# Kernel optimization log

Measured on AMD Instinct MI355X. Metric: run time of the kernel, lower is better.

Reference implementation:

```python
import jax, jax.numpy as jnp
import numpy as np

DIM = 256
HEADS = 8
HID = 4 * DIM
EPS = 1e-5


def _layernorm(x, g, b):
    mu = jnp.mean(x, axis=-1, keepdims=True)
    var = jnp.var(x, axis=-1, keepdims=True)
    return (x - mu) * jax.lax.rsqrt(var + EPS) * g + b


def setup_inputs() -> dict:
    key = jax.random.key(0)
    ks = jax.random.split(key, 16)
    s = 0.02
    return {
        "x": jax.random.normal(ks[0], (8, DIM, 32, 32), jnp.float32),
        "ln1_g": jnp.ones((DIM,), jnp.float32),
        "ln1_b": jnp.zeros((DIM,), jnp.float32),
        "wqkv": jax.random.normal(ks[1], (3 * DIM, DIM), jnp.float32) * s,
        "bqkv": jnp.zeros((3 * DIM,), jnp.float32),
        "wo": jax.random.normal(ks[2], (DIM, DIM), jnp.float32) * s,
        "bo": jnp.zeros((DIM,), jnp.float32),
        "ln2_g": jnp.ones((DIM,), jnp.float32),
        "ln2_b": jnp.zeros((DIM,), jnp.float32),
        "w1": jax.random.normal(ks[3], (HID, DIM), jnp.float32) * s,
        "b1": jnp.zeros((HID,), jnp.float32),
        "w2": jax.random.normal(ks[4], (DIM, HID), jnp.float32) * s,
        "b2": jnp.zeros((DIM,), jnp.float32),
        "c1_w": jax.random.normal(ks[5], (DIM, DIM), jnp.float32) * s,
        "c1_b": jnp.zeros((DIM,), jnp.float32),
        "c2_w": jax.random.normal(ks[6], (DIM, DIM), jnp.float32) * s,
        "c2_b": jnp.zeros((DIM,), jnp.float32),
        "c3_w": jax.random.normal(ks[7], (DIM, DIM), jnp.float32) * s,
        "c3_b": jnp.zeros((DIM,), jnp.float32),
        "dw_w": jax.random.normal(ks[8], (DIM, 1, 3, 3), jnp.float32) * s,
        "dw_b": jnp.zeros((DIM,), jnp.float32),
    }


def _block(x, ln1_g, ln1_b, wqkv, bqkv, wo, bo, ln2_g, ln2_b,
           w1, b1, w2, b2, c1_w, c1_b, c2_w, c2_b, c3_w, c3_b, dw_w, dw_b):
    b, c, h, w = x.shape
    s = h * w
    t = x.reshape(b, c, s).transpose(0, 2, 1)  # [b, s, c]

    # --- MHA sublayer ---
    tn = _layernorm(t, ln1_g, ln1_b)
    qkv = tn @ wqkv.T + bqkv                    # [b, s, 3c]
    q, k, v = jnp.split(qkv, 3, axis=-1)
    d = c // HEADS
    q = q.reshape(b, s, HEADS, d)
    k = k.reshape(b, s, HEADS, d)
    v = v.reshape(b, s, HEADS, d)
    scores = jnp.einsum("bshd,bthd->bhst", q, k) / jnp.sqrt(jnp.float32(d))
    attn = jax.nn.softmax(scores, axis=-1)
    o = jnp.einsum("bhst,bthd->bshd", attn, v).reshape(b, s, c)
    t = t + (o @ wo.T + bo)

    # --- MLP sublayer ---
    tn = _layernorm(t, ln2_g, ln2_b)
    hdn = jax.nn.gelu(tn @ w1.T + b1, approximate=False)
    t = t + (hdn @ w2.T + b2)

    x2 = t.transpose(0, 2, 1).reshape(b, c, h, w)

    # --- FeatureDenoiser: channel-attention ([b,c,c]) + depthwise gaussian ---
    def conv1x1(z, wgt, bias):
        return jnp.einsum("oc,bchw->bohw", wgt, z) + bias[None, :, None, None]

    qf = conv1x1(x2, c1_w, c1_b).reshape(b, c, s)
    kf = conv1x1(x2, c2_w, c2_b).reshape(b, c, s)
    vf = conv1x1(x2, c3_w, c3_b).reshape(b, c, s)
    a = jax.nn.softmax(jnp.einsum("bcs,bds->bcd", qf, kf), axis=-1)  # [b,c,c]
    den = jnp.einsum("bcd,bds->bcs", a, vf).reshape(b, c, h, w)
    local = jax.lax.conv_general_dilated(
        x2, dw_w, window_strides=(1, 1), padding="SAME",
        dimension_numbers=("NCHW", "OIHW", "NCHW"),
        feature_group_count=c) + dw_b[None, :, None, None]
    return x2 + 0.1 * den + 0.1 * local


def reference(x, ln1_g, ln1_b, wqkv, bqkv, wo, bo, ln2_g, ln2_b,
              w1, b1, w2, b2, c1_w, c1_b, c2_w, c2_b, c3_w, c3_b, dw_w, dw_b):
    return _block(x, ln1_g, ln1_b, wqkv, bqkv, wo, bo, ln2_g, ln2_b,
                  w1, b1, w2, b2, c1_w, c1_b, c2_w, c2_b, c3_w, c3_b, dw_w, dw_b)
```

## Files before the change

### kernel.cpp

```cpp
#include <hip/hip_runtime.h>
#include <hip/hip_bf16.h>
#include <math.h>

#define B_   8
#define C_   256
#define S_   1024
#define M_   8192
#define HID_ 1024
#define NELT 2097152

typedef __attribute__((ext_vector_type(4))) float f32x4;
typedef __attribute__((ext_vector_type(8))) short bf16x8;

__device__ __forceinline__ ushort f2bf(float f) {
  union { float f; unsigned u; } c; c.f = f;
  unsigned u = c.u;
  return (ushort)((u + 0x7fff + ((u >> 16) & 1)) >> 16);
}
__device__ __forceinline__ ushort f2bf_fast(float f) {
  __hip_bfloat16 h = __float2bfloat16(f);
  return *reinterpret_cast<ushort*>(&h);
}
__device__ __forceinline__ float bf2f(ushort u) {
  union { unsigned u; float f; } c;
  c.u = ((unsigned)u) << 16;
  return c.f;
}

__device__ __forceinline__ float waveReduceSum(float v) {
#pragma unroll
  for (int off = 32; off > 0; off >>= 1) v += __shfl_xor(v, off);
  return v;
}

__global__ __launch_bounds__(512) void ln1_tiled(const float* __restrict__ x,
                                                 const float* __restrict__ g,
                                                 const float* __restrict__ bta,
                                                 float* __restrict__ t,
                                                 ushort* __restrict__ tn) {
  __shared__ float T[32][257];
  __shared__ float mus[32], rss[32];
  int blk = blockIdx.x;
  int st = blk & 31, b = blk >> 5;
  int tid = threadIdx.x;
  int s0 = st * 32;
  for (int i = tid; i < 2048; i += 512) {
    int c = i >> 3, j4 = (i & 7) * 4;
    float4 v = *(const float4*)&x[((size_t)(b * 256 + c) << 10) + s0 + j4];
    T[j4 + 0][c] = v.x; T[j4 + 1][c] = v.y;
    T[j4 + 2][c] = v.z; T[j4 + 3][c] = v.w;
  }
  __syncthreads();
  {
    int j = tid >> 4, e = tid & 15;
    float s1 = 0.f, s2 = 0.f;
#pragma unroll
    for (int cc = 0; cc < 16; ++cc) {
      float v = T[j][e + cc * 16];
      s1 += v; s2 += v * v;
    }
    s1 += __shfl_xor(s1, 1); s2 += __shfl_xor(s2, 1);
    s1 += __shfl_xor(s1, 2); s2 += __shfl_xor(s2, 2);
    s1 += __shfl_xor(s1, 4); s2 += __shfl_xor(s2, 4);
    s1 += __shfl_xor(s1, 8); s2 += __shfl_xor(s2, 8);
    if (e == 0) {
      float mu = s1 * (1.0f / 256.0f);
      float var = s2 * (1.0f / 256.0f) - mu * mu;
      mus[j] = mu;
      rss[j] = rsqrtf(var + 1e-5f);
    }
  }
  __syncthreads();
  for (int i = tid; i < 4096; i += 512) {
    int jj = i >> 7, c = (i & 127) * 2;
    float mu = mus[jj], rs = rss[jj];
    float v0 = T[jj][c], v1 = T[jj][c + 1];
    size_t row = (size_t)(b * 1024 + s0 + jj) * 256 + c;
    float2 tv = {v0, v1};
    *(float2*)&t[row] = tv;
    uint pk = (uint)f2bf((v0 - mu) * rs * g[c] + bta[c]) |
              ((uint)f2bf((v1 - mu) * rs * g[c + 1] + bta[c + 1]) << 16);
    *(uint*)&tn[row] = pk;
  }
}

__global__ __launch_bounds__(256) void ln_kernel(const float* __restrict__ in,
                                                 const float* __restrict__ g,
                                                 const float* __restrict__ bta,
                                                 ushort* __restrict__ tn) {
  int wave = threadIdx.x >> 6, lane = threadIdx.x & 63;
  int row = blockIdx.x * 4 + wave;
  float4 v = *(const float4*)&in[(size_t)row * 256 + lane * 4];
  float s1 = (v.x + v.y) + (v.z + v.w);
  float s2 = (v.x * v.x + v.y * v.y) + (v.z * v.z + v.w * v.w);
#pragma unroll
  for (int off = 32; off > 0; off >>= 1) {
    s1 += __shfl_xor(s1, off);
    s2 += __shfl_xor(s2, off);
  }
  float mu = s1 * (1.0f / 256.0f);
  float var = s2 * (1.0f / 256.0f) - mu * mu;
  float rs = rsqrtf(var + 1e-5f);
  float4 gv = *(const float4*)&g[lane * 4];
  float4 bv = *(const float4*)&bta[lane * 4];
  uint2 pk;
  pk.x = (uint)f2bf((v.x - mu) * rs * gv.x + bv.x) |
         ((uint)f2bf((v.y - mu) * rs * gv.y + bv.y) << 16);
  pk.y = (uint)f2bf((v.z - mu) * rs * gv.z + bv.z) |
         ((uint)f2bf((v.w - mu) * rs * gv.w + bv.w) << 16);
  *(uint2*)&tn[(size_t)row * 256 + lane * 4] = pk;
}

__global__ __launch_bounds__(256) void cvt_all(
    const float* __restrict__ s0, const float* __restrict__ s1,
    const float* __restrict__ s2, const float* __restrict__ s3,
    const float* __restrict__ s4, const float* __restrict__ s5,
    const float* __restrict__ s6, const float* __restrict__ b0,
    const float* __restrict__ b1, const float* __restrict__ b2,
    ushort* __restrict__ dst, float* __restrict__ dstb) {
  int i = blockIdx.x * 256 + threadIdx.x;
  if (i < 983040) {
    const float* s; int off;
    if (i < 196608)      { s = s0; off = 0; }
    else if (i < 262144) { s = s1; off = 196608; }
    else if (i < 524288) { s = s2; off = 262144; }
    else if (i < 786432) { s = s3; off = 524288; }
    else if (i < 851968) { s = s4; off = 786432; }
    else if (i < 917504) { s = s5; off = 851968; }
    else                 { s = s6; off = 917504; }
    dst[i] = f2bf(s[i - off]);
  } else {
    int j = i - 983040;
    dstb[j] = j < 256 ? b0[j] : (j < 512 ? b1[j - 256] : b2[j - 512]);
  }
}

__device__ __forceinline__ int swzr(int r) { return (r ^ (r >> 2)) & 3; }
__device__ __forceinline__ float gelu_exact(float v) {
  return 0.5f * v * (1.0f + erff(v * 0.70710678118654752f));
}

template <int MF, int ACT, int EPI, int BROW>
__global__ __launch_bounds__(256) void gemm_t(
    const ushort* __restrict__ A, const ushort* __restrict__ W,
    const float* __restrict__ bias, const float* __restrict__ res,
    float* __restrict__ Cf, ushort* __restrict__ Cb, void* __restrict__ Cx,
    void* __restrict__ Cx2, int M, int Nn, int K,
    int a_rpb, long long a_bstride, int w_rpb, long long w_bstride) {
  __shared__ ushort As[MF * 2048];
  __shared__ ushort Bs[2048];
  int tid = threadIdx.x;
  int lane = tid & 63, wave = tid >> 6;
  int m0 = blockIdx.y * (MF * 64), n0 = blockIdx.x * 64;
  int kz = blockIdx.z;
  int Kp = K / (int)gridDim.z;
  int kbeg = kz * Kp;
  if (EPI == 0 && Cf) Cf += (size_t)kz * ((size_t)M * Nn);
  const ushort* Ab;
  if (a_rpb)
    Ab = A + (size_t)(m0 / a_rpb) * a_bstride + (size_t)(m0 % a_rpb) * K;
  else
    Ab = A + (size_t)m0 * K;
  const ushort* Wb = W + (size_t)n0 * K;
  if (w_rpb) Wb += (size_t)(m0 / w_rpb) * w_bstride;
  int srow = tid >> 2;
  int sch = tid & 3;
  int fr = lane & 15, fh = lane >> 4;
  int wr = wave * (MF * 16);
  f32x4 acc[MF][4];
#pragma unroll
  for (int i = 0; i < MF; ++i)
#pragma unroll
    for (int j = 0; j < 4; ++j) acc[i][j] = (f32x4){0.f, 0.f, 0.f, 0.f};

  int sw0 = (sch ^ swzr(srow)) * 8;
  int sw1 = (sch ^ swzr(srow + 64)) * 8;
  for (int k0 = kbeg; k0 < kbeg + Kp; k0 += 32) {
    uint4 a0 = *(const uint4*)&Ab[(size_t)srow * K + k0 + sch * 8];
    uint4 a1;
    if (MF == 2) a1 = *(const uint4*)&Ab[(size_t)(srow + 64) * K + k0 + sch * 8];
    uint4 b0 = *(const uint4*)&Wb[(size_t)srow * K + k0 + sch * 8];
    __syncthreads();
    *(uint4*)&As[srow * 32 + sw0] = a0;
    if (MF == 2) *(uint4*)&As[(srow + 64) * 32 + sw1] = a1;
    *(uint4*)&Bs[srow * 32 + sw0] = b0;
    __syncthreads();
    bf16x8 af[MF], bfv[4];
#pragma unroll
    for (int mi = 0; mi < MF; ++mi) {
      int r = wr + mi * 16 + fr;
      af[mi] = *(const bf16x8*)&As[r * 32 + ((fh ^ swzr(r)) * 8)];
    }
#pragma unroll
    for (int ni = 0; ni < 4; ++ni) {
      int r = ni * 16 + fr;
      bfv[ni] = *(const bf16x8*)&Bs[r * 32 + ((fh ^ swzr(r)) * 8)];
    }
#pragma unroll
    for (int mi = 0; mi < MF; ++mi)
#pragma unroll
      for (int ni = 0; ni < 4; ++ni)
        acc[mi][ni] = __builtin_amdgcn_mfma_f32_16x16x32_bf16(
            af[mi], bfv[ni], acc[mi][ni], 0, 0, 0);
  }
#pragma unroll
  for (int mi = 0; mi < MF; ++mi) {
    int rowb = m0 + wr + mi * 16 + fh * 4;
#pragma unroll
    for (int ni = 0; ni < 4; ++ni) {
      int col = n0 + ni * 16 + fr;
      float bv = 0.f;
      if (bias && !BROW) bv = bias[col];
      float vals[4];
#pragma unroll
      for (int r = 0; r < 4; ++r) {
        int row = rowb + r;
        float v = acc[mi][ni][r];
        if (bias && BROW) bv = bias[row & 255];
        v += bv;
        if (ACT == 1) v = gelu_exact(v);
        if (res) v += res[(size_t)row * Nn + col];
        vals[r] = v;
      }
      if (EPI == 0) {
#pragma unroll
        for (int r = 0; r < 4; ++r)
          Cf[(size_t)(rowb + r) * Nn + col] = vals[r];
      } else if (EPI == 1) {
#pragma unroll
        for (int r = 0; r < 4; ++r)
          Cb[(size_t)(rowb + r) * Nn + col] = f2bf(vals[r]);
      } else if (EPI == 3) {
        int bb = rowb >> 10;
        int s0v = rowb & 1023;
        if (col < 256) {
#pragma unroll
          for (int r = 0; r < 4; ++r)
            Cb[(size_t)(rowb + r) * 256 + col] = f2bf(vals[r]);
        } else if (col < 512) {
          int d = col - 256, hh = d >> 5, dh = d & 31;
          ushort* kfr = (ushort*)Cx;
          size_t base = ((size_t)(bb * 8 + hh) * 64 + (s0v >> 4)) * 512 +
                        (dh >> 3) * 128 + (dh & 7) + (s0v & 15) * 8;
#pragma unroll
          for (int r = 0; r < 4; ++r) kfr[base + r * 8] = f2bf(vals[r]);
        } else {
          int d = col - 512, hh = d >> 5, dh = d & 31;
          int chunk = s0v >> 5, lg = (s0v >> 3) & 3;
          int lr = dh & 15, half = dh >> 4;
          ushort* vfr = (ushort*)Cx2;
          size_t base = ((size_t)(bb * 8 + hh) * 64 + chunk * 2 + half) * 512 +
                        (lr + 16 * lg) * 8 + (s0v & 7);
          uint2 pk;
          pk.x = (uint)f2bf(vals[0]) | ((uint)f2bf(vals[1]) << 16);
          pk.y = (uint)f2bf(vals[2]) | ((uint)f2bf(vals[3]) << 16);
          *(uint2*)&vfr[base] = pk;
        }
      } else if (EPI == 4) {
#pragma unroll
        for (int r = 0; r < 4; ++r)
          Cb[(size_t)(rowb + r) * Nn + col] = f2bf(vals[r]);
        float4 v4 = {vals[0], vals[1], vals[2], vals[3]};
        float* x2p = (float*)Cx;
        *(float4*)&x2p[((size_t)((rowb >> 10) * 256 + col)) * 1024 +
                       (rowb & 1023)] = v4;
      } else if (EPI == 5) {
        if (col < 512) {
          uint2 pk;
          pk.x = (uint)f2bf(vals[0]) | ((uint)f2bf(vals[1]) << 16);
          pk.y = (uint)f2bf(vals[2]) | ((uint)f2bf(vals[3]) << 16);
          ushort* qk = (ushort*)Cx;
          *(uint2*)&qk[(size_t)(col >> 8) * 2097152 +
                       (((size_t)(rowb >> 10) * 256 + (col & 255)) << 10) +
                       (rowb & 1023)] = pk;
        } else {
#pragma unroll
          for (int r = 0; r < 4; ++r)
            Cb[(size_t)(rowb + r) * 256 + (col - 512)] = f2bf(vals[r]);
        }
      }
    }
  }
}

__global__ __launch_bounds__(256, 4) void attn_mfma(const ushort* __restrict__ q_bf,
                                                    const ushort* __restrict__ kfrag,
                                                    const ushort* __restrict__ vfrag,
                                                    ushort* __restrict__ o) {
  __shared__ ushort P[4][16][136];
  int blk = blockIdx.x;
  int qt = (blk >> 3) & 15;
  int bh = ((blk & 7) << 3) | (blk >> 7);
  int b = bh >> 3, h = bh & 7;
  int tid = threadIdx.x, wave = tid >> 6, lane = tid & 63;
  int lr = lane & 15, lg = lane >> 4;
  int q0 = qt * 64 + wave * 16;
  bf16x8 qf = *(const bf16x8*)&q_bf[(size_t)((b << 10) + q0 + lr) * 256 +
                                    h * 32 + lg * 8];
  const ushort* kbase = kfrag + (size_t)bh * 32768 + lane * 8;
  const ushort* vbase = vfrag + (size_t)bh * 32768 + lane * 8;
  ushort* Prow = &P[wave][lr][0];
  int xs = lr & 7;
  f32x4 o0 = {0.f, 0.f, 0.f, 0.f}, o1 = {0.f, 0.f, 0.f, 0.f};
  float lsum = 0.f;
  const float scale = 0.17677669529663687f;
  const f32x4 zero = {0.f, 0.f, 0.f, 0.f};

  bf16x8 kf[8];
#pragma unroll
  for (int i = 0; i < 8; ++i)
    kf[i] = *(const bf16x8*)&kbase[(size_t)i * 512];

  for (int t = 0; t < 8; ++t) {
    f32x4 s[8];
    __builtin_amdgcn_s_setprio(1);
#pragma unroll
    for (int i = 0; i < 8; ++i)
      s[i] = __builtin_amdgcn_mfma_f32_16x16x32_bf16(kf[i], qf, zero, 0, 0, 0);
    __builtin_amdgcn_s_setprio(0);
    bf16x8 v0f[4], v1f[4];
#pragma unroll
    for (int kc = 0; kc < 4; ++kc) {
      v0f[kc] = *(const bf16x8*)&vbase[(size_t)((t * 4 + kc) * 2) * 512];
      v1f[kc] = *(const bf16x8*)&vbase[(size_t)((t * 4 + kc) * 2 + 1) * 512];
    }
    if (t < 7) {
#pragma unroll
      for (int i = 0; i < 8; ++i)
        kf[i] = *(const bf16x8*)&kbase[(size_t)((t + 1) * 8 + i) * 512];
    }
    float ps = 0.f;
#pragma unroll
    for (int i = 0; i < 8; ++i) {
      float p0 = __expf(fminf(s[i][0] * scale, 30.f));
      float p1 = __expf(fminf(s[i][1] * scale, 30.f));
      float p2 = __expf(fminf(s[i][2] * scale, 30.f));
      float p3 = __expf(fminf(s[i][3] * scale, 30.f));
      ps += (p0 + p1) + (p2 + p3);
      uint2 pk;
      pk.x = (uint)f2bf_fast(p0) | ((uint)f2bf_fast(p1) << 16);
      pk.y = (uint)f2bf_fast(p2) | ((uint)f2bf_fast(p3) << 16);
      *(uint2*)&Prow[((i ^ xs) * 16) + lg * 4] = pk;
    }
    lsum += ps;
    __builtin_amdgcn_s_setprio(1);
#pragma unroll
    for (int kc4 = 0; kc4 < 4; ++kc4) {
      bf16x8 pf = *(const bf16x8*)&Prow[((kc4 * 8 + lg * 2) ^ (xs * 4)) * 4];
      o0 = __builtin_amdgcn_mfma_f32_16x16x32_bf16(v0f[kc4], pf, o0, 0, 0, 0);
      o1 = __builtin_amdgcn_mfma_f32_16x16x32_bf16(v1f[kc4], pf, o1, 0, 0, 0);
    }
    __builtin_amdgcn_s_setprio(0);
  }
  float lf = lsum + __shfl_xor(lsum, 16);
  lf += __shfl_xor(lf, 32);
  float inv = 1.f / lf;
  uint2 pk0, pk1;
  pk0.x = (uint)f2bf_fast(o0[0] * inv) | ((uint)f2bf_fast(o0[1] * inv) << 16);
  pk0.y = (uint)f2bf_fast(o0[2] * inv) | ((uint)f2bf_fast(o0[3] * inv) << 16);
  pk1.x = (uint)f2bf_fast(o1[0] * inv) | ((uint)f2bf_fast(o1[1] * inv) << 16);
  pk1.y = (uint)f2bf_fast(o1[2] * inv) | ((uint)f2bf_fast(o1[3] * inv) << 16);
  ushort* orow = &o[(size_t)((b << 10) + q0 + lr) * 256 + h * 32];
  *(uint2*)&orow[lg * 4] = pk0;
  *(uint2*)&orow[16 + lg * 4] = pk1;
}

template <int KS>
__global__ __launch_bounds__(256) void softmax256(const float* __restrict__ a,
                                                  ushort* __restrict__ ab) {
  __shared__ float s1s[4];
  int row = blockIdx.x;
  int j = threadIdx.x;
  float v = 0.f;
#pragma unroll
  for (int p = 0; p < KS; ++p) v += a[(size_t)p * 524288 + row * 256 + j];
  float mx = v;
#pragma unroll
  for (int off = 32; off > 0; off >>= 1) mx = fmaxf(mx, __shfl_xor(mx, off));
  int wave = threadIdx.x >> 6;
  if ((threadIdx.x & 63) == 0) s1s[wave] = mx;
  __syncthreads();
  mx = fmaxf(fmaxf(s1s[0], s1s[1]), fmaxf(s1s[2], s1s[3]));
  __syncthreads();
  float e = __expf(v - mx);
  float ss = waveReduceSum(e);
  if ((threadIdx.x & 63) == 0) s1s[wave] = ss;
  __syncthreads();
  ss = s1s[0] + s1s[1] + s1s[2] + s1s[3];
  ab[(size_t)row * 256 + j] = f2bf(e / ss);
}

__global__ __launch_bounds__(256) void final_kernel(
    const float* __restrict__ x2, const ushort* __restrict__ den_bf,
    const float* __restrict__ dww, const float* __restrict__ dwb,
    float* __restrict__ out) {
  int idx = blockIdx.x * 256 + threadIdx.x;
  int s = idx & 1023;
  int c = (idx >> 10) & 255;
  int b = idx >> 18;
  int y = s >> 5, x = s & 31;
  const float* plane = x2 + (size_t)(b * C_ + c) * S_;
  float lsum = 0.f;
#pragma unroll
  for (int dy = -1; dy <= 1; ++dy) {
    int yy = y + dy;
    if (yy < 0 || yy > 31) continue;
#pragma unroll
    for (int dx = -1; dx <= 1; ++dx) {
      int xx = x + dx;
      if (xx < 0 || xx > 31) continue;
      lsum += dww[c * 9 + (dy + 1) * 3 + (dx + 1)] * plane[yy * 32 + xx];
    }
  }
  lsum += dwb[c];
  out[idx] = x2[idx] + 0.1f * bf2f(den_bf[idx]) + 0.1f * lsum;
}

extern "C" void kernel_launch(void* const* d_in, const int* in_sizes, int n_in,
                              void* d_out, int out_size, void* d_ws,
                              size_t ws_size, hipStream_t stream) {
  const float* x     = (const float*)d_in[0];
  const float* ln1_g = (const float*)d_in[1];
  const float* ln1_b = (const float*)d_in[2];
  const float* wqkv  = (const float*)d_in[3];
  const float* bqkv  = (const float*)d_in[4];
  const float* wo    = (const float*)d_in[5];
  const float* bo    = (const float*)d_in[6];
  const float* ln2_g = (const float*)d_in[7];
  const float* ln2_b = (const float*)d_in[8];
  const float* w1    = (const float*)d_in[9];
  const float* b1    = (const float*)d_in[10];
  const float* w2f   = (const float*)d_in[11];
  const float* b2    = (const float*)d_in[12];
  const float* c1_w  = (const float*)d_in[13];
  const float* c1_b  = (const float*)d_in[14];
  const float* c2_w  = (const float*)d_in[15];
  const float* c2_b  = (const float*)d_in[16];
  const float* c3_w  = (const float*)d_in[17];
  const float* c3_b  = (const float*)d_in[18];
  const float* dw_w  = (const float*)d_in[19];
  const float* dw_b  = (const float*)d_in[20];
  float* out = (float*)d_out;

  float* ws = (float*)d_ws;
  const size_t N = NELT;
  float* t        = ws;
  ushort* q_bf    = (ushort*)(ws + N);
  ushort* kfrag   = (ushort*)(ws + N + N / 2);
  ushort* vfrag   = (ushort*)(ws + 2 * N);
  ushort* hdn_bf  = (ushort*)(ws + N);
  float* amat4    = ws + N;
  ushort* tn_bf   = (ushort*)(ws + 3 * N);
  ushort* o_bf    = (ushort*)(ws + 3 * N + N / 2);
  float* x2       = ws + 4 * N;
  ushort* den_bf  = (ushort*)(ws + 5 * N);
  ushort* t_bf    = (ushort*)(ws + 6 * N);
  ushort* qf_c    = (ushort*)(ws + 6 * N + N / 2);
  ushort* kf_c    = (ushort*)(ws + 7 * N);
  ushort* vf      = (ushort*)(ws + 7 * N + N / 2);
  float* cbias    = ws + 8 * N;
  ushort* amat_bf = (ushort*)(ws + 8 * N + N / 4);
  ushort* wbf     = (ushort*)(ws + 8 * N + N / 2);
  ushort* wqkv_bf = wbf;
  ushort* wo_bf   = wbf + 196608;
  ushort* w1_bf   = wbf + 262144;
  ushort* w2_bf   = wbf + 524288;
  ushort* c123_bf = wbf + 786432;

  const long long PB = 262144;

  cvt_all<<<3843, 256, 0, stream>>>(wqkv, wo, w1, w2f, c1_w, c2_w, c3_w, c1_b,
                                    c2_b, c3_b, wbf, cbias);
  ln1_tiled<<<256, 512, 0, stream>>>(x, ln1_g, ln1_b, t, tn_bf);
  gemm_t<1, 0, 3, 0><<<dim3(12, 128), 256, 0, stream>>>(
      tn_bf, wqkv_bf, bqkv, nullptr, nullptr, q_bf, kfrag, vfrag, M_, 768, 256,
      0, 0, 0, 0);
  attn_mfma<<<1024, 256, 0, stream>>>(q_bf, kfrag, vfrag, o_bf);
  gemm_t<1, 0, 0, 0><<<dim3(4, 128), 256, 0, stream>>>(
      o_bf, wo_bf, bo, t, t, nullptr, nullptr, nullptr, M_, 256, 256, 0, 0, 0,
      0);
  ln_kernel<<<2048, 256, 0, stream>>>(t, ln2_g, ln2_b, tn_bf);
  gemm_t<1, 1, 1, 0><<<dim3(16, 128), 256, 0, stream>>>(
      tn_bf, w1_bf, b1, nullptr, nullptr, hdn_bf, nullptr, nullptr, M_, HID_,
      256, 0, 0, 0, 0);
  gemm_t<1, 0, 4, 0><<<dim3(4, 128), 256, 0, stream>>>(
      hdn_bf, w2_bf, b2, t, nullptr, t_bf, x2, nullptr, M_, 256, HID_, 0, 0, 0,
      0);
  gemm_t<1, 0, 5, 0><<<dim3(12, 128), 256, 0, stream>>>(
      t_bf, c123_bf, cbias, nullptr, nullptr, vf, qf_c, nullptr, M_, 768, 256,
      0, 0, 0, 0);
  gemm_t<1, 0, 0, 0><<<dim3(4, 32, 4), 256, 0, stream>>>(
      qf_c, kf_c, nullptr, nullptr, amat4, nullptr, nullptr, nullptr, 2048,
      256, 1024, 256, PB, 256, PB);
  softmax256<4><<<2048, 256, 0, stream>>>(amat4, amat_bf);
  gemm_t<1, 0, 1, 0><<<dim3(16, 32), 256, 0, stream>>>(
      amat_bf, vf, nullptr, nullptr, nullptr, den_bf, nullptr, nullptr, 2048,
      1024, 256, 0, 0, 256, PB);
  final_kernel<<<8192, 256, 0, stream>>>(x2, den_bf, dw_w, dw_b, out);
}
```

Before: 154.9 us.

## Fuse weight conversion into LN1 prep and fuse Wo GEMM with LN2

Merges the weight/bias bf16 conversion kernel into the LN1 transpose kernel, so one launch covers both through extra blocks. Replaces the Wo-projection GEMM and the separate LN2 kernel with one kernel. Each block computes a full 16-row by 256-column output tile, adds bias and residual, and applies LayerNorm from shared memory. This removes a launch and a round trip of the residual stream through global memory. In exchange, the fused GEMM uses small 16-row tiles and reloads the whole 256x256 weight per block, which may lower MFMA efficiency.

```diff
diff --git a/kernel.cpp b/kernel.cpp
--- a/kernel.cpp
+++ b/kernel.cpp
@@ -33,30 +33,152 @@
   return v;
 }
 
-__global__ __launch_bounds__(512) void ln1_tiled(const float* __restrict__ x,
-                                                 const float* __restrict__ g,
-                                                 const float* __restrict__ bta,
-                                                 float* __restrict__ t,
-                                                 ushort* __restrict__ tn) {
+__global__ __launch_bounds__(512) void prep_kernel(
+    const float* __restrict__ x, const float* __restrict__ g,
+    const float* __restrict__ bta, float* __restrict__ t,
+    ushort* __restrict__ tn,
+    const float* __restrict__ s0, const float* __restrict__ s1,
+    const float* __restrict__ s2, const float* __restrict__ s3,
+    const float* __restrict__ s4, const float* __restrict__ s5,
+    const float* __restrict__ s6, const float* __restrict__ b0,
+    const float* __restrict__ b1, const float* __restrict__ b2,
+    ushort* __restrict__ wdst, float* __restrict__ bdst) {
   __shared__ float T[32][257];
   __shared__ float mus[32], rss[32];
   int blk = blockIdx.x;
+  int tid = threadIdx.x;
+  if (blk >= 256) {
+    int i = (blk - 256) * 512 + tid;
+    if (i < 983040) {
+      const float* s; int off;
+      if (i < 196608)      { s = s0; off = 0; }
+      else if (i < 262144) { s = s1; off = 196608; }
+      else if (i < 524288) { s = s2; off = 262144; }
+      else if (i < 786432) { s = s3; off = 524288; }
+      else if (i < 851968) { s = s4; off = 786432; }
+      else if (i < 917504) { s = s5; off = 851968; }
+      else                 { s = s6; off = 917504; }
+      wdst[i] = f2bf(s[i - off]);
+    } else if (i < 983808) {
+      int j = i - 983040;
+      bdst[j] = j < 256 ? b0[j] : (j < 512 ? b1[j - 256] : b2[j - 512]);
+    }
+    return;
+  }
   int st = blk & 31, b = blk >> 5;
-  int tid = threadIdx.x;
-  int s0 = st * 32;
+  int s0i = st * 32;
   for (int i = tid; i < 2048; i += 512) {
     int c = i >> 3, j4 = (i & 7) * 4;
-    float4 v = *(const float4*)&x[((size_t)(b * 256 + c) << 10) + s0 + j4];
+    float4 v = *(const float4*)&x[((size_t)(b * 256 + c) << 10) + s0i + j4];
     T[j4 + 0][c] = v.x; T[j4 + 1][c] = v.y;
     T[j4 + 2][c] = v.z; T[j4 + 3][c] = v.w;
   }
   __syncthreads();
   {
     int j = tid >> 4, e = tid & 15;
-    float s1 = 0.f, s2 = 0.f;
+    float s1v = 0.f, s2v = 0.f;
 #pragma unroll
     for (int cc = 0; cc < 16; ++cc) {
       float v = T[j][e + cc * 16];
+      s1v += v; s2v += v * v;
+    }
+    s1v += __shfl_xor(s1v, 1); s2v += __shfl_xor(s2v, 1);
+    s1v += __shfl_xor(s1v, 2); s2v += __shfl_xor(s2v, 2);
+    s1v += __shfl_xor(s1v, 4); s2v += __shfl_xor(s2v, 4);
+    s1v += __shfl_xor(s1v, 8); s2v += __shfl_xor(s2v, 8);
+    if (e == 0) {
+      float mu = s1v * (1.0f / 256.0f);
+      float var = s2v * (1.0f / 256.0f) - mu * mu;
+      mus[j] = mu;
+      rss[j] = rsqrtf(var + 1e-5f);
+    }
+  }
+  __syncthreads();
+  for (int i = tid; i < 4096; i += 512) {
+    int jj = i >> 7, c = (i & 127) * 2;
+    float mu = mus[jj], rs = rss[jj];
+    float v0 = T[jj][c], v1 = T[jj][c + 1];
+    size_t row = (size_t)(b * 1024 + s0i + jj) * 256 + c;
+    float2 tv = {v0, v1};
+    *(float2*)&t[row] = tv;
+    uint pk = (uint)f2bf((v0 - mu) * rs * g[c] + bta[c]) |
+              ((uint)f2bf((v1 - mu) * rs * g[c + 1] + bta[c + 1]) << 16);
+    *(uint*)&tn[row] = pk;
+  }
+}
+
+__device__ __forceinline__ int swzr(int r) { return (r ^ (r >> 2)) & 3; }
+__device__ __forceinline__ float gelu_exact(float v) {
+  return 0.5f * v * (1.0f + erff(v * 0.70710678118654752f));
+}
+
+__global__ __launch_bounds__(256) void gemm_wo_ln(
+    const ushort* __restrict__ A, const ushort* __restrict__ W,
+    const float* __restrict__ bias, const float* __restrict__ res,
+    float* __restrict__ tout, ushort* __restrict__ tn,
+    const float* __restrict__ g, const float* __restrict__ bta) {
+  __shared__ ushort As[512];
+  __shared__ ushort Bs[8192];
+  __shared__ float F[16][257];
+  __shared__ float mus[16], rss[16];
+  int tid = threadIdx.x;
+  int lane = tid & 63, wave = tid >> 6;
+  int m0 = blockIdx.x * 16;
+  int fr = lane & 15, fh = lane >> 4;
+  int srow = tid >> 2, sch = tid & 3;
+  f32x4 acc[4];
+#pragma unroll
+  for (int j = 0; j < 4; ++j) acc[j] = (f32x4){0.f, 0.f, 0.f, 0.f};
+
+  for (int k0 = 0; k0 < 256; k0 += 32) {
+    uint4 bb0 = *(const uint4*)&W[(size_t)srow * 256 + k0 + sch * 8];
+    uint4 bb1 = *(const uint4*)&W[(size_t)(srow + 64) * 256 + k0 + sch * 8];
+    uint4 bb2 = *(const uint4*)&W[(size_t)(srow + 128) * 256 + k0 + sch * 8];
+    uint4 bb3 = *(const uint4*)&W[(size_t)(srow + 192) * 256 + k0 + sch * 8];
+    uint4 aa;
+    if (tid < 64)
+      aa = *(const uint4*)&A[(size_t)(m0 + (tid >> 2)) * 256 + k0 +
+                             (tid & 3) * 8];
+    __syncthreads();
+    *(uint4*)&Bs[srow * 32 + ((sch ^ swzr(srow)) * 8)] = bb0;
+    *(uint4*)&Bs[(srow + 64) * 32 + ((sch ^ swzr(srow + 64)) * 8)] = bb1;
+    *(uint4*)&Bs[(srow + 128) * 32 + ((sch ^ swzr(srow + 128)) * 8)] = bb2;
+    *(uint4*)&Bs[(srow + 192) * 32 + ((sch ^ swzr(srow + 192)) * 8)] = bb3;
+    if (tid < 64)
+      *(uint4*)&As[(tid >> 2) * 32 + (((tid & 3) ^ swzr(tid >> 2)) * 8)] = aa;
+    __syncthreads();
+    bf16x8 af = *(const bf16x8*)&As[fr * 32 + ((fh ^ swzr(fr)) * 8)];
+    bf16x8 bfv[4];
+#pragma unroll
+    for (int ni = 0; ni < 4; ++ni) {
+      int rrow = wave * 64 + ni * 16 + fr;
+      bfv[ni] = *(const bf16x8*)&Bs[rrow * 32 + ((fh ^ swzr(rrow)) * 8)];
+    }
+#pragma unroll
+    for (int ni = 0; ni < 4; ++ni)
+      acc[ni] = __builtin_amdgcn_mfma_f32_16x16x32_bf16(af, bfv[ni], acc[ni],
+                                                        0, 0, 0);
+  }
+#pragma unroll
+  for (int ni = 0; ni < 4; ++ni) {
+    int col = wave * 64 + ni * 16 + fr;
+    float bv = bias[col];
+#pragma unroll
+    for (int r = 0; r < 4; ++r) {
+      int rowl = fh * 4 + r;
+      int row = m0 + rowl;
+      float v = acc[ni][r] + bv + res[(size_t)row * 256 + col];
+      tout[(size_t)row * 256 + col] = v;
+      F[rowl][col] = v;
+    }
+  }
+  __syncthreads();
+  {
+    int rowl = tid >> 4, e = tid & 15;
+    float s1 = 0.f, s2 = 0.f;
+#pragma unroll
+    for (int k = 0; k < 16; ++k) {
+      float v = F[rowl][e + k * 16];
       s1 += v; s2 += v * v;
     }
     s1 += __shfl_xor(s1, 1); s2 += __shfl_xor(s2, 1);
@@ -66,78 +188,19 @@
     if (e == 0) {
       float mu = s1 * (1.0f / 256.0f);
       float var = s2 * (1.0f / 256.0f) - mu * mu;
-      mus[j] = mu;
-      rss[j] = rsqrtf(var + 1e-5f);
-    }
-  }
-  __syncthreads();
-  for (int i = tid; i < 4096; i += 512) {
-    int jj = i >> 7, c = (i & 127) * 2;
-    float mu = mus[jj], rs = rss[jj];
-    float v0 = T[jj][c], v1 = T[jj][c + 1];
-    size_t row = (size_t)(b * 1024 + s0 + jj) * 256 + c;
-    float2 tv = {v0, v1};
-    *(float2*)&t[row] = tv;
+      mus[rowl] = mu;
+      rss[rowl] = rsqrtf(var + 1e-5f);
+    }
+  }
+  __syncthreads();
+  for (int i = tid; i < 2048; i += 256) {
+    int rowl = i >> 7, c = (i & 127) * 2;
+    float mu = mus[rowl], rs = rss[rowl];
+    float v0 = F[rowl][c], v1 = F[rowl][c + 1];
     uint pk = (uint)f2bf((v0 - mu) * rs * g[c] + bta[c]) |
               ((uint)f2bf((v1 - mu) * rs * g[c + 1] + bta[c + 1]) << 16);
-    *(uint*)&tn[row] = pk;
-  }
-}
-
-__global__ __launch_bounds__(256) void ln_kernel(const float* __restrict__ in,
-                                                 const float* __restrict__ g,
-                                                 const float* __restrict__ bta,
-                                                 ushort* __restrict__ tn) {
-  int wave = threadIdx.x >> 6, lane = threadIdx.x & 63;
-  int row = blockIdx.x * 4 + wave;
-  float4 v = *(const float4*)&in[(size_t)row * 256 + lane * 4];
-  float s1 = (v.x + v.y) + (v.z + v.w);
-  float s2 = (v.x * v.x + v.y * v.y) + (v.z * v.z + v.w * v.w);
-#pragma unroll
-  for (int off = 32; off > 0; off >>= 1) {
-    s1 += __shfl_xor(s1, off);
-    s2 += __shfl_xor(s2, off);
-  }
-  float mu = s1 * (1.0f / 256.0f);
-  float var = s2 * (1.0f / 256.0f) - mu * mu;
-  float rs = rsqrtf(var + 1e-5f);
-  float4 gv = *(const float4*)&g[lane * 4];
-  float4 bv = *(const float4*)&bta[lane * 4];
-  uint2 pk;
-  pk.x = (uint)f2bf((v.x - mu) * rs * gv.x + bv.x) |
-         ((uint)f2bf((v.y - mu) * rs * gv.y + bv.y) << 16);
-  pk.y = (uint)f2bf((v.z - mu) * rs * gv.z + bv.z) |
-         ((uint)f2bf((v.w - mu) * rs * gv.w + bv.w) << 16);
-  *(uint2*)&tn[(size_t)row * 256 + lane * 4] = pk;
-}
-
-__global__ __launch_bounds__(256) void cvt_all(
-    const float* __restrict__ s0, const float* __restrict__ s1,
-    const float* __restrict__ s2, const float* __restrict__ s3,
-    const float* __restrict__ s4, const float* __restrict__ s5,
-    const float* __restrict__ s6, const float* __restrict__ b0,
-    const float* __restrict__ b1, const float* __restrict__ b2,
-    ushort* __restrict__ dst, float* __restrict__ dstb) {
-  int i = blockIdx.x * 256 + threadIdx.x;
-  if (i < 983040) {
-    const float* s; int off;
-    if (i < 196608)      { s = s0; off = 0; }
-    else if (i < 262144) { s = s1; off = 196608; }
-    else if (i < 524288) { s = s2; off = 262144; }
-    else if (i < 786432) { s = s3; off = 524288; }
-    else if (i < 851968) { s = s4; off = 786432; }
-    else if (i < 917504) { s = s5; off = 851968; }
-    else                 { s = s6; off = 917504; }
-    dst[i] = f2bf(s[i - off]);
-  } else {
-    int j = i - 983040;
-    dstb[j] = j < 256 ? b0[j] : (j < 512 ? b1[j - 256] : b2[j - 512]);
-  }
-}
-
-__device__ __forceinline__ int swzr(int r) { return (r ^ (r >> 2)) & 3; }
-__device__ __forceinline__ float gelu_exact(float v) {
-  return 0.5f * v * (1.0f + erff(v * 0.70710678118654752f));
+    *(uint*)&tn[(size_t)(m0 + rowl) * 256 + c] = pk;
+  }
 }
 
 template <int MF, int ACT, int EPI, int BROW>
@@ -469,17 +532,15 @@
 
   const long long PB = 262144;
 
-  cvt_all<<<3843, 256, 0, stream>>>(wqkv, wo, w1, w2f, c1_w, c2_w, c3_w, c1_b,
-                                    c2_b, c3_b, wbf, cbias);
-  ln1_tiled<<<256, 512, 0, stream>>>(x, ln1_g, ln1_b, t, tn_bf);
+  prep_kernel<<<2178, 512, 0, stream>>>(x, ln1_g, ln1_b, t, tn_bf, wqkv, wo,
+                                        w1, w2f, c1_w, c2_w, c3_w, c1_b, c2_b,
+                                        c3_b, wbf, cbias);
   gemm_t<1, 0, 3, 0><<<dim3(12, 128), 256, 0, stream>>>(
       tn_bf, wqkv_bf, bqkv, nullptr, nullptr, q_bf, kfrag, vfrag, M_, 768, 256,
       0, 0, 0, 0);
   attn_mfma<<<1024, 256, 0, stream>>>(q_bf, kfrag, vfrag, o_bf);
-  gemm_t<1, 0, 0, 0><<<dim3(4, 128), 256, 0, stream>>>(
-      o_bf, wo_bf, bo, t, t, nullptr, nullptr, nullptr, M_, 256, 256, 0, 0, 0,
-      0);
-  ln_kernel<<<2048, 256, 0, stream>>>(t, ln2_g, ln2_b, tn_bf);
+  gemm_wo_ln<<<512, 256, 0, stream>>>(o_bf, wo_bf, bo, t, t, tn_bf, ln2_g,
+                                      ln2_b);
   gemm_t<1, 1, 1, 0><<<dim3(16, 128), 256, 0, stream>>>(
       tn_bf, w1_bf, b1, nullptr, nullptr, hdn_bf, nullptr, nullptr, M_, HID_,
       256, 0, 0, 0, 0);
```

Measured after the change: 146.7 us. 5.3% less time.
